# Kernel tuning notes

Hardware: AMD Instinct MI355X
Metric: run time of the kernel (lower is better)

The kernel has to match this reference:

```python
import jax, jax.numpy as jnp
import numpy as np

B, N, L, E, U, G, R, C = 128, 50000, 8, 250000, 10000, 20000, 2000, 2


def setup_inputs() -> dict:
    key = jax.random.key(0)
    k1, k2, k3, k4, k5, k6 = jax.random.split(key, 6)
    rng = np.random.default_rng(0)
    # unique index sets (scatter .set requires unique targets for determinism)
    gene_map = jnp.asarray(rng.permutation(N)[:G].astype(np.int64))
    dst_unique = jnp.asarray(np.stack([rng.permutation(N)[:U] for _ in range(L)]).astype(np.int64))
    root_ids = jnp.asarray(rng.permutation(N)[:R].astype(np.int64))
    return {
        "X_gene_batch": jax.random.normal(k1, (B, G), dtype=jnp.float32),
        "layer_weight": 0.01 * jnp.ones((L,), dtype=jnp.float32),
        "node_bias": 0.1 * jax.random.normal(k2, (N,), dtype=jnp.float32),
        "head_W": jax.random.normal(k3, (C, R), dtype=jnp.float32) / np.sqrt(R),
        "head_b": jnp.zeros((C,), dtype=jnp.float32),
        "gene_map": gene_map,
        "src": jax.random.randint(k4, (L, E), 0, N, dtype=jnp.int64),
        "dst_pos": jax.random.randint(k5, (L, E), 0, U, dtype=jnp.int64),
        "dst_unique": dst_unique,
        "root_ids": root_ids,
    }


def reference(X_gene_batch, layer_weight, node_bias, head_W, head_b,
              gene_map, src, dst_pos, dst_unique, root_ids):
    B_, dtype = X_gene_batch.shape[0], X_gene_batch.dtype
    N_ = node_bias.shape[0]
    L_, _ = src.shape
    U_ = dst_unique.shape[1]
    # init scalar state: h[:, gene_map] = X
    h = jnp.zeros((B_, N_), dtype=dtype).at[:, gene_map].set(X_gene_batch)
    for li in range(L_):  # small fixed layer loop (structurally distinct steps)
        msg = h[:, src[li]] * layer_weight[li]                      # [B, E] gather + scale
        agg = jnp.zeros((B_, U_), dtype=dtype).at[:, dst_pos[li]].add(msg)  # segment sum
        h_dst = jnp.tanh(agg + node_bias[dst_unique[li]][None, :])  # bias + tanh (dropout=0)
        h = h.at[:, dst_unique[li]].set(h_dst)                      # scatter write back
    feat = h[:, root_ids]                                           # [B, R] roots concat
    return feat @ head_W.T + head_b                                 # [B, C]
```

## Files before the change

kernel.cpp:

```cpp
#include <hip/hip_runtime.h>

constexpr int Bb = 128;
constexpr int Nn = 50000;
constexpr int Ll = 8;
constexpr int Ee = 250000;
constexpr int Uu = 10000;
constexpr int Gg = 20000;
constexpr int Rr = 2000;
constexpr int Cc = 2;

constexpr int NB1 = 40;
constexpr int BW1 = 256;
constexpr int CAP = 7424;
constexpr int CH2 = 256;
constexpr int RIT = Uu * 32;

typedef __attribute__((ext_vector_type(2))) float f32x2;


__device__ __forceinline__ float b2f(unsigned short x) {
    return __uint_as_float((unsigned)x << 16);
}
__device__ __forceinline__ unsigned short f2b(float f) {
    unsigned u = __float_as_uint(f);
    return (unsigned short)((u + 0x7FFFu + ((u >> 16) & 1u)) >> 16);
}
__device__ __forceinline__ unsigned pkbf(float a, float b) {
    return (unsigned)f2b(a) | ((unsigned)f2b(b) << 16);
}

__global__ void zero_kernel(unsigned int* __restrict__ hz, unsigned int* __restrict__ h8z,
                            unsigned int* __restrict__ pz, int* __restrict__ gcur) {
    int idx = blockIdx.x * blockDim.x + threadIdx.x;
    if (idx < Nn * 64) hz[idx] = 0u;
    if (idx < Nn * 32) h8z[idx] = 0u;
    if (idx < Ll * Nn / 2) pz[idx] = 0xFFFFFFFFu;
    if (idx < Ll * NB1) gcur[idx] = 0;
}

__global__ __launch_bounds__(256) void genes_kernel(const float* __restrict__ X,
                                                    const int* __restrict__ gmap,
                                                    const int* __restrict__ dstu,
                                                    unsigned short* __restrict__ h,
                                                    unsigned int* __restrict__ h8,
                                                    unsigned short* __restrict__ postab) {
    int gt = blockIdx.x * 256 + (int)threadIdx.x;
    if (gt < Ll * Uu) {
        int li = gt / Uu;
        postab[(size_t)li * Nn + dstu[gt]] = (unsigned short)(gt - li * Uu);
    }
    int g0 = blockIdx.x * 32;
    __shared__ float tile[32][129];
    #pragma unroll
    for (int i = 0; i < 16; ++i) {
        int idx = i * 256 + (int)threadIdx.x;
        int gl = idx & 31, b = idx >> 5;
        tile[gl][b] = X[(size_t)b * Gg + g0 + gl];
    }
    __syncthreads();
    #pragma unroll
    for (int i = 0; i < 16; ++i) {
        int idx = i * 256 + (int)threadIdx.x;
        int b = idx & 127, gl = idx >> 7;
        h[(size_t)gmap[g0 + gl] * Bb + b] = f2b(tile[gl][b]);
    }
    #pragma unroll
    for (int i = 0; i < 4; ++i) {
        int idx = i * 256 + (int)threadIdx.x;
        int q = idx & 31, gl = idx >> 5;
        int node = gmap[g0 + gl];
        int w8 = __builtin_amdgcn_cvt_pk_fp8_f32(tile[gl][q * 4 + 0], tile[gl][q * 4 + 1], 0, false);
        w8 = __builtin_amdgcn_cvt_pk_fp8_f32(tile[gl][q * 4 + 2], tile[gl][q * 4 + 3], w8, true);
        h8[(size_t)node * 32 + q] = (unsigned int)w8;
    }
}

__global__ __launch_bounds__(256) void part_kernel(const int* __restrict__ src,
                                                   const int* __restrict__ dstp,
                                                   int* __restrict__ gcur,
                                                   unsigned int* __restrict__ region) {
    int li = blockIdx.x / CH2, ch = blockIdx.x % CH2;
    const int ePer = (Ee + CH2 - 1) / CH2;
    int e0 = ch * ePer, e1 = min(e0 + ePer, Ee);
    const int* s = src + (size_t)li * Ee;
    const int* d = dstp + (size_t)li * Ee;

    __shared__ int hist[NB1];
    __shared__ int base[NB1];
    __shared__ int cur[NB1];
    if (threadIdx.x < NB1) { hist[threadIdx.x] = 0; cur[threadIdx.x] = 0; }
    __syncthreads();

    for (int e = e0 + (int)threadIdx.x; e < e1; e += 256)
        atomicAdd(&hist[d[e] >> 8], 1);
    __syncthreads();

    if (threadIdx.x < NB1) {
        int c = hist[threadIdx.x];
        base[threadIdx.x] = (c > 0) ? atomicAdd(&gcur[li * NB1 + (int)threadIdx.x], c) : 0;
    }
    __syncthreads();

    for (int e = e0 + (int)threadIdx.x; e < e1; e += 256) {
        int dd = d[e];
        int bkt = dd >> 8;
        unsigned int packed = ((unsigned int)s[e] << 8) | (unsigned int)(dd & 255);
        int pos = base[bkt] + atomicAdd(&cur[bkt], 1);
        region[((size_t)li * NB1 + bkt) * CAP + pos] = packed;
    }
}

__global__ __launch_bounds__(256) void emit_kernel(const unsigned int* __restrict__ region,
                                                   const int* __restrict__ gcur,
                                                   const unsigned short* __restrict__ postab,
                                                   unsigned int* __restrict__ ssrc,
                                                   int* __restrict__ rp) {
    int li = blockIdx.x / NB1, b = blockIdx.x % NB1;
    int n = gcur[li * NB1 + b];
    const unsigned int* r = region + ((size_t)li * NB1 + b) * CAP;
    __shared__ int hh[BW1];
    __shared__ int ofs[BW1];
    __shared__ int sbase;
    __shared__ unsigned short lout[CAP];
    if (threadIdx.x < BW1) hh[threadIdx.x] = 0;
    if (threadIdx.x < 64) {
        int t = threadIdx.x;
        int v = (t < NB1) ? gcur[li * NB1 + t] : 0;
        int sc = v;
        #pragma unroll
        for (int off = 1; off < 64; off <<= 1) {
            int x = __shfl_up(sc, (unsigned)off, 64);
            if (t >= off) sc += x;
        }
        if (t == b) sbase = sc - v;
        if (b == NB1 - 1 && t == NB1 - 1) rp[li * (Uu + 1) + Uu] = sc;
    }
    __syncthreads();
    for (int i = threadIdx.x; i < n; i += 256) atomicAdd(&hh[r[i] & 255], 1);
    __syncthreads();
    if (threadIdx.x < 64) {
        int carry = 0;
        #pragma unroll
        for (int c = 0; c < BW1 / 64; ++c) {
            int v = hh[c * 64 + (int)threadIdx.x];
            int sc = v;
            #pragma unroll
            for (int off = 1; off < 64; off <<= 1) {
                int x = __shfl_up(sc, (unsigned)off, 64);
                if ((int)threadIdx.x >= off) sc += x;
            }
            ofs[c * 64 + (int)threadIdx.x] = carry + sc - v;
            carry += __shfl(sc, 63, 64);
        }
    }
    __syncthreads();
    int base = sbase;
    if (threadIdx.x < BW1) {
        int dg = b * BW1 + (int)threadIdx.x;
        if (dg < Uu) rp[li * (Uu + 1) + dg] = base + ofs[threadIdx.x];
    }
    __syncthreads();
    for (int i = threadIdx.x; i < n; i += 256) {
        unsigned int p = r[i];
        int pos = atomicAdd(&ofs[p & 255], 1);
        lout[pos] = (unsigned short)(p >> 8);
    }
    __syncthreads();
    unsigned int* o = ssrc + (size_t)li * Ee + base;
    if (li == 0) {
        for (int i = threadIdx.x; i < n; i += 256) o[i] = lout[i];
    } else {
        const unsigned short* pt = postab + (size_t)(li - 1) * Nn;
        unsigned int soff = (unsigned)(Nn + ((li - 1) & 1) * Uu);
        for (int i = threadIdx.x; i < n; i += 256) {
            unsigned short s = lout[i];
            unsigned short p = pt[s];
            o[i] = (p != 0xFFFFu) ? (soff + (unsigned)p) : (unsigned)s;
        }
    }
}

__global__ __launch_bounds__(256) void layer_fused(unsigned short* h,
                                                   unsigned int* h8,
                                                   const unsigned int* __restrict__ ssrc,
                                                   const int* __restrict__ rp,
                                                   const int* __restrict__ dstu,
                                                   const float* __restrict__ lw,
                                                   const float* __restrict__ bias,
                                                   int li) {
    int idx = blockIdx.x * 256 + (int)threadIdx.x;
    if (idx < RIT) {
        int u = idx >> 5;
        int lane5 = idx & 31;
        int sub = lane5 >> 3;
        int l8 = lane5 & 7;
        int beg = rp[u], end = rp[u + 1];
        const uint4* hp = (const uint4*)h8;
        float acc[16];
        #pragma unroll
        for (int j = 0; j < 16; ++j) acc[j] = 0.f;
        f32x2 p;
        int k = beg + sub;
        for (; k + 4 < end; k += 8) {
            unsigned s0 = ssrc[k], s1 = ssrc[k + 4];
            uint4 v0 = hp[(size_t)s0 * 8 + l8];
            uint4 v1 = hp[(size_t)s1 * 8 + l8];
            p = __builtin_amdgcn_cvt_pk_f32_fp8(v0.x, false); acc[0] += p.x;  acc[1] += p.y;
            p = __builtin_amdgcn_cvt_pk_f32_fp8(v0.x, true);  acc[2] += p.x;  acc[3] += p.y;
            p = __builtin_amdgcn_cvt_pk_f32_fp8(v0.y, false); acc[4] += p.x;  acc[5] += p.y;
            p = __builtin_amdgcn_cvt_pk_f32_fp8(v0.y, true);  acc[6] += p.x;  acc[7] += p.y;
            p = __builtin_amdgcn_cvt_pk_f32_fp8(v0.z, false); acc[8] += p.x;  acc[9] += p.y;
            p = __builtin_amdgcn_cvt_pk_f32_fp8(v0.z, true);  acc[10] += p.x; acc[11] += p.y;
            p = __builtin_amdgcn_cvt_pk_f32_fp8(v0.w, false); acc[12] += p.x; acc[13] += p.y;
            p = __builtin_amdgcn_cvt_pk_f32_fp8(v0.w, true);  acc[14] += p.x; acc[15] += p.y;
            p = __builtin_amdgcn_cvt_pk_f32_fp8(v1.x, false); acc[0] += p.x;  acc[1] += p.y;
            p = __builtin_amdgcn_cvt_pk_f32_fp8(v1.x, true);  acc[2] += p.x;  acc[3] += p.y;
            p = __builtin_amdgcn_cvt_pk_f32_fp8(v1.y, false); acc[4] += p.x;  acc[5] += p.y;
            p = __builtin_amdgcn_cvt_pk_f32_fp8(v1.y, true);  acc[6] += p.x;  acc[7] += p.y;
            p = __builtin_amdgcn_cvt_pk_f32_fp8(v1.z, false); acc[8] += p.x;  acc[9] += p.y;
            p = __builtin_amdgcn_cvt_pk_f32_fp8(v1.z, true);  acc[10] += p.x; acc[11] += p.y;
            p = __builtin_amdgcn_cvt_pk_f32_fp8(v1.w, false); acc[12] += p.x; acc[13] += p.y;
            p = __builtin_amdgcn_cvt_pk_f32_fp8(v1.w, true);  acc[14] += p.x; acc[15] += p.y;
        }
        if (k < end) {
            uint4 v0 = hp[(size_t)ssrc[k] * 8 + l8];
            p = __builtin_amdgcn_cvt_pk_f32_fp8(v0.x, false); acc[0] += p.x;  acc[1] += p.y;
            p = __builtin_amdgcn_cvt_pk_f32_fp8(v0.x, true);  acc[2] += p.x;  acc[3] += p.y;
            p = __builtin_amdgcn_cvt_pk_f32_fp8(v0.y, false); acc[4] += p.x;  acc[5] += p.y;
            p = __builtin_amdgcn_cvt_pk_f32_fp8(v0.y, true);  acc[6] += p.x;  acc[7] += p.y;
            p = __builtin_amdgcn_cvt_pk_f32_fp8(v0.z, false); acc[8] += p.x;  acc[9] += p.y;
            p = __builtin_amdgcn_cvt_pk_f32_fp8(v0.z, true);  acc[10] += p.x; acc[11] += p.y;
            p = __builtin_amdgcn_cvt_pk_f32_fp8(v0.w, false); acc[12] += p.x; acc[13] += p.y;
            p = __builtin_amdgcn_cvt_pk_f32_fp8(v0.w, true);  acc[14] += p.x; acc[15] += p.y;
        }
        #pragma unroll
        for (int j = 0; j < 16; ++j) {
            acc[j] += __shfl_xor(acc[j], 8, 64);
            acc[j] += __shfl_xor(acc[j], 16, 64);
        }
        if (sub == 0) {
            float wv = lw[li];
            float bs = bias[dstu[li * Uu + u]];
            float t[16];
            #pragma unroll
            for (int j = 0; j < 16; ++j) t[j] = tanhf(acc[j] * wv + bs);
            size_t srow = (size_t)(Nn + (li & 1) * Uu + u);
            uint4 o0, o1;
            o0.x = pkbf(t[0], t[1]);   o0.y = pkbf(t[2], t[3]);
            o0.z = pkbf(t[4], t[5]);   o0.w = pkbf(t[6], t[7]);
            o1.x = pkbf(t[8], t[9]);   o1.y = pkbf(t[10], t[11]);
            o1.z = pkbf(t[12], t[13]); o1.w = pkbf(t[14], t[15]);
            *(uint4*)(h + srow * Bb + l8 * 16) = o0;
            *(uint4*)(h + srow * Bb + l8 * 16 + 8) = o1;
            uint4 of;
            int w8;
            w8 = __builtin_amdgcn_cvt_pk_fp8_f32(t[0], t[1], 0, false);
            w8 = __builtin_amdgcn_cvt_pk_fp8_f32(t[2], t[3], w8, true);   of.x = (unsigned)w8;
            w8 = __builtin_amdgcn_cvt_pk_fp8_f32(t[4], t[5], 0, false);
            w8 = __builtin_amdgcn_cvt_pk_fp8_f32(t[6], t[7], w8, true);   of.y = (unsigned)w8;
            w8 = __builtin_amdgcn_cvt_pk_fp8_f32(t[8], t[9], 0, false);
            w8 = __builtin_amdgcn_cvt_pk_fp8_f32(t[10], t[11], w8, true); of.z = (unsigned)w8;
            w8 = __builtin_amdgcn_cvt_pk_fp8_f32(t[12], t[13], 0, false);
            w8 = __builtin_amdgcn_cvt_pk_fp8_f32(t[14], t[15], w8, true); of.w = (unsigned)w8;
            *(uint4*)(h8 + srow * 32 + l8 * 4) = of;
        }
    } else if (li > 0) {
        int j = idx - RIT;
        if (j >= RIT) return;
        int u = j >> 5, lane = j & 31;
        int node = dstu[(li - 1) * Uu + u];
        size_t srow = (size_t)(Nn + ((li - 1) & 1) * Uu + u);
        *(ushort4*)(h + (size_t)node * Bb + lane * 4) =
            *(const ushort4*)(h + srow * Bb + lane * 4);
        h8[(size_t)node * 32 + lane] = h8[srow * 32 + lane];
    }
}

__global__ void head_kernel(const unsigned short* __restrict__ h,
                            const unsigned short* __restrict__ postab,
                            const int* __restrict__ roots,
                            const float* __restrict__ W, const float* __restrict__ hb,
                            float* __restrict__ out) {
    int b = blockIdx.x;
    int t = threadIdx.x;
    const unsigned short* pt = postab + (size_t)7 * Nn;
    float a0 = 0.f, a1 = 0.f;
    for (int r = t; r < Rr; r += 256) {
        int node = roots[r];
        unsigned short p = pt[node];
        int row = (p != 0xFFFFu) ? (Nn + Uu + (int)p) : node;
        float v = b2f(h[(size_t)row * Bb + b]);
        a0 += v * W[r];
        a1 += v * W[Rr + r];
    }
    __shared__ float s0[256], s1[256];
    s0[t] = a0; s1[t] = a1;
    __syncthreads();
    for (int off = 128; off > 0; off >>= 1) {
        if (t < off) { s0[t] += s0[t + off]; s1[t] += s1[t + off]; }
        __syncthreads();
    }
    if (t == 0) {
        out[b * Cc + 0] = s0[0] + hb[0];
        out[b * Cc + 1] = s1[0] + hb[1];
    }
}

extern "C" void kernel_launch(void* const* d_in, const int* in_sizes, int n_in,
                              void* d_out, int out_size, void* d_ws, size_t ws_size,
                              hipStream_t stream) {
    const float* X      = (const float*)d_in[0];
    const float* lw     = (const float*)d_in[1];
    const float* bias   = (const float*)d_in[2];
    const float* headW  = (const float*)d_in[3];
    const float* headb  = (const float*)d_in[4];
    const int*   gmap   = (const int*)d_in[5];
    const int*   src    = (const int*)d_in[6];
    const int*   dstp   = (const int*)d_in[7];
    const int*   dstu   = (const int*)d_in[8];
    const int*   roots  = (const int*)d_in[9];
    float* out = (float*)d_out;

    char* w = (char*)d_ws;
    unsigned short* h_t    = (unsigned short*)w; w += (size_t)(Nn + 2 * Uu) * Bb * 2;
    unsigned int*   h8     = (unsigned int*)w;   w += (size_t)(Nn + 2 * Uu) * Bb;
    unsigned int*   region = (unsigned int*)w;   w += (size_t)Ll * NB1 * CAP * 4;
    unsigned int*   ssrc   = (unsigned int*)w;   w += (size_t)Ll * Ee * 4;
    int*            rp     = (int*)w;            w += (size_t)Ll * (Uu + 1) * 4;
    unsigned short* postab = (unsigned short*)w; w += (size_t)Ll * Nn * 2;
    int*            gcur   = (int*)w;            w += (size_t)Ll * NB1 * 4;

    const int BLK = 256;

    zero_kernel<<<(Nn * 64 + BLK - 1) / BLK, BLK, 0, stream>>>(
        (unsigned int*)h_t, h8, (unsigned int*)postab, gcur);
    genes_kernel<<<Gg / 32, BLK, 0, stream>>>(X, gmap, dstu, h_t, h8, postab);

    part_kernel<<<Ll * CH2, BLK, 0, stream>>>(src, dstp, gcur, region);
    emit_kernel<<<Ll * NB1, BLK, 0, stream>>>(region, gcur, postab, ssrc, rp);

    for (int li = 0; li < Ll; ++li) {
        int items = RIT + (li > 0 ? RIT : 0);
        layer_fused<<<(items + BLK - 1) / BLK, BLK, 0, stream>>>(
            h_t, h8, ssrc + (size_t)li * Ee, rp + (size_t)li * (Uu + 1),
            dstu, lw, bias, li);
    }

    head_kernel<<<Bb, 256, 0, stream>>>(h_t, postab, roots, headW, headb, out);
}
```

Measured before the change: 151.1 us.

## Use per-layer staging rows for fp8 state and drop deferred write-back pass

Each layer now writes its fp8 output to a dedicated staging slot (one per layer) instead of a two-slot ping-pong buffer. A new rowof table, built once from postab, resolves each source node to its latest staging row for every layer. The bf16 state is written directly to the destination node rows. This removes the copy-back half of every layer launch and the postab lookup in the head, at the cost of a larger fp8 workspace and an extra rowof precompute kernel and table. Gathers now read from rows spread over more memory, which may reduce cache locality.

```diff
diff --git a/kernel.cpp b/kernel.cpp
--- a/kernel.cpp
+++ b/kernel.cpp
@@ -14,6 +14,7 @@
 constexpr int CAP = 7424;
 constexpr int CH2 = 256;
 constexpr int RIT = Uu * 32;
+constexpr int NSTG = 7;
 
 typedef __attribute__((ext_vector_type(2))) float f32x2;
 
@@ -75,6 +76,20 @@
     }
 }
 
+__global__ void rowof_kernel(const unsigned short* __restrict__ postab,
+                             unsigned int* __restrict__ rowof) {
+    int n = blockIdx.x * 256 + (int)threadIdx.x;
+    if (n >= Nn) return;
+    unsigned r = (unsigned)n;
+    rowof[n] = r;
+    #pragma unroll
+    for (int li = 1; li < Ll; ++li) {
+        unsigned short p = postab[(size_t)(li - 1) * Nn + n];
+        if (p != 0xFFFFu) r = (unsigned)(Nn + (li - 1) * Uu + (int)p);
+        rowof[(size_t)li * Nn + n] = r;
+    }
+}
+
 __global__ __launch_bounds__(256) void part_kernel(const int* __restrict__ src,
                                                    const int* __restrict__ dstp,
                                                    int* __restrict__ gcur,
@@ -112,7 +127,7 @@
 
 __global__ __launch_bounds__(256) void emit_kernel(const unsigned int* __restrict__ region,
                                                    const int* __restrict__ gcur,
-                                                   const unsigned short* __restrict__ postab,
+                                                   const unsigned int* __restrict__ rowof,
                                                    unsigned int* __restrict__ ssrc,
                                                    int* __restrict__ rp) {
     int li = blockIdx.x / NB1, b = blockIdx.x % NB1;
@@ -167,91 +182,83 @@
     }
     __syncthreads();
     unsigned int* o = ssrc + (size_t)li * Ee + base;
-    if (li == 0) {
-        for (int i = threadIdx.x; i < n; i += 256) o[i] = lout[i];
-    } else {
-        const unsigned short* pt = postab + (size_t)(li - 1) * Nn;
-        unsigned int soff = (unsigned)(Nn + ((li - 1) & 1) * Uu);
-        for (int i = threadIdx.x; i < n; i += 256) {
-            unsigned short s = lout[i];
-            unsigned short p = pt[s];
-            o[i] = (p != 0xFFFFu) ? (soff + (unsigned)p) : (unsigned)s;
-        }
-    }
-}
-
-__global__ __launch_bounds__(256) void layer_fused(unsigned short* h,
-                                                   unsigned int* h8,
-                                                   const unsigned int* __restrict__ ssrc,
-                                                   const int* __restrict__ rp,
-                                                   const int* __restrict__ dstu,
-                                                   const float* __restrict__ lw,
-                                                   const float* __restrict__ bias,
-                                                   int li) {
+    const unsigned int* ro = rowof + (size_t)li * Nn;
+    for (int i = threadIdx.x; i < n; i += 256) o[i] = ro[lout[i]];
+}
+
+__global__ __launch_bounds__(256) void layer_kernel(unsigned short* __restrict__ h,
+                                                    unsigned int* __restrict__ h8,
+                                                    const unsigned int* __restrict__ ssrc,
+                                                    const int* __restrict__ rp,
+                                                    const int* __restrict__ dstu,
+                                                    const float* __restrict__ lw,
+                                                    const float* __restrict__ bias,
+                                                    int li) {
     int idx = blockIdx.x * 256 + (int)threadIdx.x;
-    if (idx < RIT) {
-        int u = idx >> 5;
-        int lane5 = idx & 31;
-        int sub = lane5 >> 3;
-        int l8 = lane5 & 7;
-        int beg = rp[u], end = rp[u + 1];
-        const uint4* hp = (const uint4*)h8;
-        float acc[16];
+    if (idx >= RIT) return;
+    int u = idx >> 5;
+    int lane5 = idx & 31;
+    int sub = lane5 >> 3;
+    int l8 = lane5 & 7;
+    int beg = rp[u], end = rp[u + 1];
+    const uint4* hp = (const uint4*)h8;
+    float acc[16];
+    #pragma unroll
+    for (int j = 0; j < 16; ++j) acc[j] = 0.f;
+    f32x2 p;
+    int k = beg + sub;
+    for (; k + 4 < end; k += 8) {
+        unsigned s0 = ssrc[k], s1 = ssrc[k + 4];
+        uint4 v0 = hp[(size_t)s0 * 8 + l8];
+        uint4 v1 = hp[(size_t)s1 * 8 + l8];
+        p = __builtin_amdgcn_cvt_pk_f32_fp8(v0.x, false); acc[0] += p.x;  acc[1] += p.y;
+        p = __builtin_amdgcn_cvt_pk_f32_fp8(v0.x, true);  acc[2] += p.x;  acc[3] += p.y;
+        p = __builtin_amdgcn_cvt_pk_f32_fp8(v0.y, false); acc[4] += p.x;  acc[5] += p.y;
+        p = __builtin_amdgcn_cvt_pk_f32_fp8(v0.y, true);  acc[6] += p.x;  acc[7] += p.y;
+        p = __builtin_amdgcn_cvt_pk_f32_fp8(v0.z, false); acc[8] += p.x;  acc[9] += p.y;
+        p = __builtin_amdgcn_cvt_pk_f32_fp8(v0.z, true);  acc[10] += p.x; acc[11] += p.y;
+        p = __builtin_amdgcn_cvt_pk_f32_fp8(v0.w, false); acc[12] += p.x; acc[13] += p.y;
+        p = __builtin_amdgcn_cvt_pk_f32_fp8(v0.w, true);  acc[14] += p.x; acc[15] += p.y;
+        p = __builtin_amdgcn_cvt_pk_f32_fp8(v1.x, false); acc[0] += p.x;  acc[1] += p.y;
+        p = __builtin_amdgcn_cvt_pk_f32_fp8(v1.x, true);  acc[2] += p.x;  acc[3] += p.y;
+        p = __builtin_amdgcn_cvt_pk_f32_fp8(v1.y, false); acc[4] += p.x;  acc[5] += p.y;
+        p = __builtin_amdgcn_cvt_pk_f32_fp8(v1.y, true);  acc[6] += p.x;  acc[7] += p.y;
+        p = __builtin_amdgcn_cvt_pk_f32_fp8(v1.z, false); acc[8] += p.x;  acc[9] += p.y;
+        p = __builtin_amdgcn_cvt_pk_f32_fp8(v1.z, true);  acc[10] += p.x; acc[11] += p.y;
+        p = __builtin_amdgcn_cvt_pk_f32_fp8(v1.w, false); acc[12] += p.x; acc[13] += p.y;
+        p = __builtin_amdgcn_cvt_pk_f32_fp8(v1.w, true);  acc[14] += p.x; acc[15] += p.y;
+    }
+    if (k < end) {
+        uint4 v0 = hp[(size_t)ssrc[k] * 8 + l8];
+        p = __builtin_amdgcn_cvt_pk_f32_fp8(v0.x, false); acc[0] += p.x;  acc[1] += p.y;
+        p = __builtin_amdgcn_cvt_pk_f32_fp8(v0.x, true);  acc[2] += p.x;  acc[3] += p.y;
+        p = __builtin_amdgcn_cvt_pk_f32_fp8(v0.y, false); acc[4] += p.x;  acc[5] += p.y;
+        p = __builtin_amdgcn_cvt_pk_f32_fp8(v0.y, true);  acc[6] += p.x;  acc[7] += p.y;
+        p = __builtin_amdgcn_cvt_pk_f32_fp8(v0.z, false); acc[8] += p.x;  acc[9] += p.y;
+        p = __builtin_amdgcn_cvt_pk_f32_fp8(v0.z, true);  acc[10] += p.x; acc[11] += p.y;
+        p = __builtin_amdgcn_cvt_pk_f32_fp8(v0.w, false); acc[12] += p.x; acc[13] += p.y;
+        p = __builtin_amdgcn_cvt_pk_f32_fp8(v0.w, true);  acc[14] += p.x; acc[15] += p.y;
+    }
+    #pragma unroll
+    for (int j = 0; j < 16; ++j) {
+        acc[j] += __shfl_xor(acc[j], 8, 64);
+        acc[j] += __shfl_xor(acc[j], 16, 64);
+    }
+    if (sub == 0) {
+        float wv = lw[li];
+        int node = dstu[li * Uu + u];
+        float bs = bias[node];
+        float t[16];
         #pragma unroll
-        for (int j = 0; j < 16; ++j) acc[j] = 0.f;
-        f32x2 p;
-        int k = beg + sub;
-        for (; k + 4 < end; k += 8) {
-            unsigned s0 = ssrc[k], s1 = ssrc[k + 4];
-            uint4 v0 = hp[(size_t)s0 * 8 + l8];
-            uint4 v1 = hp[(size_t)s1 * 8 + l8];
-            p = __builtin_amdgcn_cvt_pk_f32_fp8(v0.x, false); acc[0] += p.x;  acc[1] += p.y;
-            p = __builtin_amdgcn_cvt_pk_f32_fp8(v0.x, true);  acc[2] += p.x;  acc[3] += p.y;
-            p = __builtin_amdgcn_cvt_pk_f32_fp8(v0.y, false); acc[4] += p.x;  acc[5] += p.y;
-            p = __builtin_amdgcn_cvt_pk_f32_fp8(v0.y, true);  acc[6] += p.x;  acc[7] += p.y;
-            p = __builtin_amdgcn_cvt_pk_f32_fp8(v0.z, false); acc[8] += p.x;  acc[9] += p.y;
-            p = __builtin_amdgcn_cvt_pk_f32_fp8(v0.z, true);  acc[10] += p.x; acc[11] += p.y;
-            p = __builtin_amdgcn_cvt_pk_f32_fp8(v0.w, false); acc[12] += p.x; acc[13] += p.y;
-            p = __builtin_amdgcn_cvt_pk_f32_fp8(v0.w, true);  acc[14] += p.x; acc[15] += p.y;
-            p = __builtin_amdgcn_cvt_pk_f32_fp8(v1.x, false); acc[0] += p.x;  acc[1] += p.y;
-            p = __builtin_amdgcn_cvt_pk_f32_fp8(v1.x, true);  acc[2] += p.x;  acc[3] += p.y;
-            p = __builtin_amdgcn_cvt_pk_f32_fp8(v1.y, false); acc[4] += p.x;  acc[5] += p.y;
-            p = __builtin_amdgcn_cvt_pk_f32_fp8(v1.y, true);  acc[6] += p.x;  acc[7] += p.y;
-            p = __builtin_amdgcn_cvt_pk_f32_fp8(v1.z, false); acc[8] += p.x;  acc[9] += p.y;
-            p = __builtin_amdgcn_cvt_pk_f32_fp8(v1.z, true);  acc[10] += p.x; acc[11] += p.y;
-            p = __builtin_amdgcn_cvt_pk_f32_fp8(v1.w, false); acc[12] += p.x; acc[13] += p.y;
-            p = __builtin_amdgcn_cvt_pk_f32_fp8(v1.w, true);  acc[14] += p.x; acc[15] += p.y;
-        }
-        if (k < end) {
-            uint4 v0 = hp[(size_t)ssrc[k] * 8 + l8];
-            p = __builtin_amdgcn_cvt_pk_f32_fp8(v0.x, false); acc[0] += p.x;  acc[1] += p.y;
-            p = __builtin_amdgcn_cvt_pk_f32_fp8(v0.x, true);  acc[2] += p.x;  acc[3] += p.y;
-            p = __builtin_amdgcn_cvt_pk_f32_fp8(v0.y, false); acc[4] += p.x;  acc[5] += p.y;
-            p = __builtin_amdgcn_cvt_pk_f32_fp8(v0.y, true);  acc[6] += p.x;  acc[7] += p.y;
-            p = __builtin_amdgcn_cvt_pk_f32_fp8(v0.z, false); acc[8] += p.x;  acc[9] += p.y;
-            p = __builtin_amdgcn_cvt_pk_f32_fp8(v0.z, true);  acc[10] += p.x; acc[11] += p.y;
-            p = __builtin_amdgcn_cvt_pk_f32_fp8(v0.w, false); acc[12] += p.x; acc[13] += p.y;
-            p = __builtin_amdgcn_cvt_pk_f32_fp8(v0.w, true);  acc[14] += p.x; acc[15] += p.y;
-        }
-        #pragma unroll
-        for (int j = 0; j < 16; ++j) {
-            acc[j] += __shfl_xor(acc[j], 8, 64);
-            acc[j] += __shfl_xor(acc[j], 16, 64);
-        }
-        if (sub == 0) {
-            float wv = lw[li];
-            float bs = bias[dstu[li * Uu + u]];
-            float t[16];
-            #pragma unroll
-            for (int j = 0; j < 16; ++j) t[j] = tanhf(acc[j] * wv + bs);
-            size_t srow = (size_t)(Nn + (li & 1) * Uu + u);
-            uint4 o0, o1;
-            o0.x = pkbf(t[0], t[1]);   o0.y = pkbf(t[2], t[3]);
-            o0.z = pkbf(t[4], t[5]);   o0.w = pkbf(t[6], t[7]);
-            o1.x = pkbf(t[8], t[9]);   o1.y = pkbf(t[10], t[11]);
-            o1.z = pkbf(t[12], t[13]); o1.w = pkbf(t[14], t[15]);
-            *(uint4*)(h + srow * Bb + l8 * 16) = o0;
-            *(uint4*)(h + srow * Bb + l8 * 16 + 8) = o1;
+        for (int j = 0; j < 16; ++j) t[j] = tanhf(acc[j] * wv + bs);
+        uint4 o0, o1;
+        o0.x = pkbf(t[0], t[1]);   o0.y = pkbf(t[2], t[3]);
+        o0.z = pkbf(t[4], t[5]);   o0.w = pkbf(t[6], t[7]);
+        o1.x = pkbf(t[8], t[9]);   o1.y = pkbf(t[10], t[11]);
+        o1.z = pkbf(t[12], t[13]); o1.w = pkbf(t[14], t[15]);
+        *(uint4*)(h + (size_t)node * Bb + l8 * 16) = o0;
+        *(uint4*)(h + (size_t)node * Bb + l8 * 16 + 8) = o1;
+        if (li < NSTG) {
             uint4 of;
             int w8;
             w8 = __builtin_amdgcn_cvt_pk_fp8_f32(t[0], t[1], 0, false);
@@ -262,34 +269,20 @@
             w8 = __builtin_amdgcn_cvt_pk_fp8_f32(t[10], t[11], w8, true); of.z = (unsigned)w8;
             w8 = __builtin_amdgcn_cvt_pk_fp8_f32(t[12], t[13], 0, false);
             w8 = __builtin_amdgcn_cvt_pk_fp8_f32(t[14], t[15], w8, true); of.w = (unsigned)w8;
-            *(uint4*)(h8 + srow * 32 + l8 * 4) = of;
+            *(uint4*)(h8 + (size_t)(Nn + li * Uu + u) * 32 + l8 * 4) = of;
         }
-    } else if (li > 0) {
-        int j = idx - RIT;
-        if (j >= RIT) return;
-        int u = j >> 5, lane = j & 31;
-        int node = dstu[(li - 1) * Uu + u];
-        size_t srow = (size_t)(Nn + ((li - 1) & 1) * Uu + u);
-        *(ushort4*)(h + (size_t)node * Bb + lane * 4) =
-            *(const ushort4*)(h + srow * Bb + lane * 4);
-        h8[(size_t)node * 32 + lane] = h8[srow * 32 + lane];
     }
 }
 
 __global__ void head_kernel(const unsigned short* __restrict__ h,
-                            const unsigned short* __restrict__ postab,
                             const int* __restrict__ roots,
                             const float* __restrict__ W, const float* __restrict__ hb,
                             float* __restrict__ out) {
     int b = blockIdx.x;
     int t = threadIdx.x;
-    const unsigned short* pt = postab + (size_t)7 * Nn;
     float a0 = 0.f, a1 = 0.f;
     for (int r = t; r < Rr; r += 256) {
-        int node = roots[r];
-        unsigned short p = pt[node];
-        int row = (p != 0xFFFFu) ? (Nn + Uu + (int)p) : node;
-        float v = b2f(h[(size_t)row * Bb + b]);
+        float v = b2f(h[(size_t)roots[r] * Bb + b]);
         a0 += v * W[r];
         a1 += v * W[Rr + r];
     }
@@ -322,12 +315,13 @@
     float* out = (float*)d_out;
 
     char* w = (char*)d_ws;
-    unsigned short* h_t    = (unsigned short*)w; w += (size_t)(Nn + 2 * Uu) * Bb * 2;
-    unsigned int*   h8     = (unsigned int*)w;   w += (size_t)(Nn + 2 * Uu) * Bb;
+    unsigned short* h_t    = (unsigned short*)w; w += (size_t)Nn * Bb * 2;
+    unsigned int*   h8     = (unsigned int*)w;   w += (size_t)(Nn + NSTG * Uu) * Bb;
     unsigned int*   region = (unsigned int*)w;   w += (size_t)Ll * NB1 * CAP * 4;
     unsigned int*   ssrc   = (unsigned int*)w;   w += (size_t)Ll * Ee * 4;
     int*            rp     = (int*)w;            w += (size_t)Ll * (Uu + 1) * 4;
     unsigned short* postab = (unsigned short*)w; w += (size_t)Ll * Nn * 2;
+    unsigned int*   rowof  = (unsigned int*)w;   w += (size_t)Ll * Nn * 4;
     int*            gcur   = (int*)w;            w += (size_t)Ll * NB1 * 4;
 
     const int BLK = 256;
@@ -335,16 +329,16 @@
     zero_kernel<<<(Nn * 64 + BLK - 1) / BLK, BLK, 0, stream>>>(
         (unsigned int*)h_t, h8, (unsigned int*)postab, gcur);
     genes_kernel<<<Gg / 32, BLK, 0, stream>>>(X, gmap, dstu, h_t, h8, postab);
+    rowof_kernel<<<(Nn + BLK - 1) / BLK, BLK, 0, stream>>>(postab, rowof);
 
     part_kernel<<<Ll * CH2, BLK, 0, stream>>>(src, dstp, gcur, region);
-    emit_kernel<<<Ll * NB1, BLK, 0, stream>>>(region, gcur, postab, ssrc, rp);
+    emit_kernel<<<Ll * NB1, BLK, 0, stream>>>(region, gcur, rowof, ssrc, rp);
 
     for (int li = 0; li < Ll; ++li) {
-        int items = RIT + (li > 0 ? RIT : 0);
-        layer_fused<<<(items + BLK - 1) / BLK, BLK, 0, stream>>>(
+        layer_kernel<<<(RIT + BLK - 1) / BLK, BLK, 0, stream>>>(
             h_t, h8, ssrc + (size_t)li * Ee, rp + (size_t)li * (Uu + 1),
             dstu, lw, bias, li);
     }
 
-    head_kernel<<<Bb, 256, 0, stream>>>(h_t, postab, roots, headW, headb, out);
-}
+    head_kernel<<<Bb, 256, 0, stream>>>(h_t, roots, headW, headb, out);
+}
```

Measured after the change: 143.2 us. 5.2% less time.
